# Optimization experiments

Measured on AMD Instinct MI355X. Metric: run time of the kernel, lower is better.

The kernel has to match this reference:

```python
import jax, jax.numpy as jnp
import numpy as np

VOCAB = 50257
EMB = 256
HID = 256
B = 128
S = 2048


def setup_inputs() -> dict:
    key = jax.random.key(0)
    ks = jax.random.split(key, 18)
    w = 0.05  # weight scale to keep tanh/sigmoid in a sane range
    return {
        "x": jax.random.randint(ks[0], (B,), 0, VOCAB),
        "encoder_states": jax.random.normal(ks[1], (S, B, HID), jnp.float32),
        "hidden": jax.random.normal(ks[2], (1, B, HID), jnp.float32),
        "cell": jax.random.normal(ks[3], (1, B, HID), jnp.float32),
        "emb_table": jax.random.normal(ks[4], (VOCAB, EMB), jnp.float32) * w,
        "W_ih": jax.random.normal(ks[5], (4 * HID, EMB + HID), jnp.float32) * w,
        "W_hh": jax.random.normal(ks[6], (4 * HID, HID), jnp.float32) * w,
        "b_ih": jax.random.normal(ks[7], (4 * HID,), jnp.float32) * w,
        "b_hh": jax.random.normal(ks[8], (4 * HID,), jnp.float32) * w,
        "fc_w": jax.random.normal(ks[9], (VOCAB, HID), jnp.float32) * w,
        "fc_b": jax.random.normal(ks[10], (VOCAB,), jnp.float32) * w,
        "W1_w": jax.random.normal(ks[11], (HID, HID), jnp.float32) * w,
        "W1_b": jax.random.normal(ks[12], (HID,), jnp.float32) * w,
        "W2_w": jax.random.normal(ks[13], (HID, HID), jnp.float32) * w,
        "W2_b": jax.random.normal(ks[14], (HID,), jnp.float32) * w,
        "V_w": jax.random.normal(ks[15], (1, HID), jnp.float32) * w,
        "V_b": jax.random.normal(ks[16], (1,), jnp.float32) * w,
    }


def reference(x, encoder_states, hidden, cell, emb_table, W_ih, W_hh, b_ih, b_hh,
              fc_w, fc_b, W1_w, W1_b, W2_w, W2_b, V_w, V_b):
    # encoder_states: [S, B, H] -> [B, S, H]
    enc = jnp.transpose(encoder_states, (1, 0, 2))
    h0 = hidden[0]  # [B, H]  (num_layers == 1)
    c0 = cell[0]

    # Bahdanau additive attention
    score = jnp.tanh(enc @ W1_w.T + W1_b + (h0 @ W2_w.T + W2_b)[:, None, :])  # [B,S,H]
    attw = jax.nn.softmax(score @ V_w.T + V_b, axis=1)  # [B, S, 1]
    ctx = jnp.sum(attw * enc, axis=1)  # [B, H]

    # embedding (dropout is identity in eval/deterministic mode)
    emb = emb_table[x]  # [B, E]
    rnn_in = jnp.concatenate([ctx, emb], axis=-1)  # [B, H+E]

    # single LSTM step; PyTorch gate order: i, f, g, o
    gates = rnn_in @ W_ih.T + b_ih + h0 @ W_hh.T + b_hh  # [B, 4H]
    i, f, g, o = jnp.split(gates, 4, axis=-1)
    c_new = jax.nn.sigmoid(f) * c0 + jax.nn.sigmoid(i) * jnp.tanh(g)
    h_new = jax.nn.sigmoid(o) * jnp.tanh(c_new)

    predictions = h_new @ fc_w.T + fc_b  # [B, VOCAB]
    return predictions, h_new[None], c_new[None], attw
```

## Files before the change

kernel.cpp:

```cpp
#include <hip/hip_runtime.h>
#include <hip/hip_bf16.h>

#define VOCAB 50257
#define EMB 256
#define HID 256
#define BB 128
#define SS 2048

typedef __attribute__((ext_vector_type(8))) short short8;
typedef __attribute__((ext_vector_type(4))) float f32x4;

__device__ inline unsigned short f2bf(float f) {
    unsigned int u = __float_as_uint(f);
    u += 0x7FFFu + ((u >> 16) & 1u);
    return (unsigned short)(u >> 16);
}
__device__ inline unsigned int pack2(float a, float b) {
    return (unsigned int)f2bf(a) | ((unsigned int)f2bf(b) << 16);
}
__device__ inline uint4 pack8(float4 a, float4 b) {
    return make_uint4(pack2(a.x, a.y), pack2(a.z, a.w), pack2(b.x, b.y), pack2(b.z, b.w));
}
__device__ inline float fast_tanh(float x) {
    x = fminf(fmaxf(x, -9.f), 9.f);
    float t = __expf(2.f * x);
    return (t - 1.f) * __builtin_amdgcn_rcpf(t + 1.f);
}

__global__ __launch_bounds__(256) void k_prep(
    const float* __restrict__ hidden, const float* __restrict__ W2,
    const float* __restrict__ W1bias, const float* __restrict__ W2bias,
    const float* __restrict__ W1, unsigned short* __restrict__ W1bf,
    float* __restrict__ qb)
{
    const int bid = blockIdx.x, tid = threadIdx.x;
    if (bid < BB) {
        __shared__ float h0s[HID];
        h0s[tid] = hidden[bid * HID + tid];
        __syncthreads();
        const float4* w2r = (const float4*)(W2 + (size_t)tid * HID);
        float acc = W1bias[tid] + W2bias[tid];
        #pragma unroll 4
        for (int k4 = 0; k4 < HID / 4; ++k4) {
            float4 w = w2r[k4];
            acc += w.x * h0s[k4*4] + w.y * h0s[k4*4+1] + w.z * h0s[k4*4+2] + w.w * h0s[k4*4+3];
        }
        qb[bid * HID + tid] = acc;
    } else {
        int idx = (bid - BB) * 256 + tid;
        float4 v = ((const float4*)W1)[idx];
        ushort4 o;
        o.x = f2bf(v.x); o.y = f2bf(v.y); o.z = f2bf(v.z); o.w = f2bf(v.w);
        ((ushort4*)W1bf)[idx] = o;
    }
}

__global__ __launch_bounds__(512, 2) void k_escore(
    const float* __restrict__ enc, const unsigned short* __restrict__ W1bf,
    const float* __restrict__ qb, const float* __restrict__ Vw,
    const float* __restrict__ Vb, float* __restrict__ e)
{
    __shared__ __align__(16) char As[256 * 128];
    __shared__ __align__(16) char Bs[256 * 128];
    __shared__ float esum[256];

    const int tid = threadIdx.x;
    const int lane = tid & 63, wid = tid >> 6;
    const int wm = wid >> 1, wn = wid & 1;
    const int lg = lane >> 4, li = lane & 15;
    const size_t row0 = (size_t)blockIdx.x * 256;

    if (tid < 256) esum[tid] = 0.f;

    f32x4 acc[4][8];
    #pragma unroll
    for (int m = 0; m < 4; ++m)
        #pragma unroll
        for (int n = 0; n < 8; ++n)
            acc[m][n] = (f32x4){0.f, 0.f, 0.f, 0.f};

    const int a_k16 = tid & 15, a_row0 = tid >> 4;
    const int b_k8 = tid & 7, b_col0 = tid >> 3;

    for (int kt = 0; kt < 4; ++kt) {
        __syncthreads();
        #pragma unroll
        for (int i = 0; i < 8; ++i) {
            const int row = a_row0 + 32 * i;
            float4 v = *((const float4*)(enc + (row0 + row) * HID + kt * 64) + a_k16);
            uint2 p = make_uint2(pack2(v.x, v.y), pack2(v.z, v.w));
            *(uint2*)(As + row * 128 + ((a_k16 * 8) ^ ((row & 7) << 4))) = p;
        }
        #pragma unroll
        for (int i = 0; i < 4; ++i) {
            const int col = b_col0 + 64 * i;
            uint4 v = *((const uint4*)(W1bf + (size_t)col * HID + kt * 64) + b_k8);
            *(uint4*)(Bs + col * 128 + ((b_k8 * 16) ^ ((col & 7) << 4))) = v;
        }
        __syncthreads();
        #pragma unroll
        for (int ks = 0; ks < 2; ++ks) {
            short8 a[4];
            #pragma unroll
            for (int m = 0; m < 4; ++m) {
                const int r = wm * 64 + m * 16 + li;
                a[m] = *(const short8*)(As + r * 128 + ((ks * 64 + lg * 16) ^ ((r & 7) << 4)));
            }
            #pragma unroll
            for (int n = 0; n < 8; ++n) {
                const int c = wn * 128 + n * 16 + li;
                short8 b = *(const short8*)(Bs + c * 128 + ((ks * 64 + lg * 16) ^ ((c & 7) << 4)));
                #pragma unroll
                for (int m = 0; m < 4; ++m)
                    acc[m][n] = __builtin_amdgcn_mfma_f32_16x16x32_bf16(a[m], b, acc[m][n], 0, 0, 0);
            }
        }
    }

    float vw[8];
    #pragma unroll
    for (int n = 0; n < 8; ++n) vw[n] = Vw[wn * 128 + n * 16 + li];

    #pragma unroll
    for (int m = 0; m < 4; ++m) {
        #pragma unroll
        for (int r = 0; r < 4; ++r) {
            const int lrow = wm * 64 + m * 16 + lg * 4 + r;
            const size_t g = row0 + lrow;
            const float* qbrow = qb + (size_t)(g & 127) * HID;
            float p = 0.f;
            #pragma unroll
            for (int n = 0; n < 8; ++n) {
                const int h = wn * 128 + n * 16 + li;
                p += vw[n] * fast_tanh(acc[m][n][r] + qbrow[h]);
            }
            p += __shfl_xor(p, 1); p += __shfl_xor(p, 2);
            p += __shfl_xor(p, 4); p += __shfl_xor(p, 8);
            if (li == 0) atomicAdd(&esum[lrow], p);
        }
    }
    __syncthreads();
    if (tid < 256) {
        const size_t g = row0 + tid;
        e[(size_t)(g & 127) * SS + (g >> 7)] = esum[tid] + Vb[0];
    }
}

__global__ __launch_bounds__(256) void k_softmax(
    const float* __restrict__ e, float* __restrict__ attw)
{
    __shared__ float redm[4];
    __shared__ float reds[4];
    const int b = blockIdx.x, tid = threadIdx.x;
    const float* er = e + (size_t)b * SS;
    float v[8];
    float m = -1e30f;
    #pragma unroll
    for (int i = 0; i < 8; ++i) { v[i] = er[tid + i * 256]; m = fmaxf(m, v[i]); }
    #pragma unroll
    for (int off = 1; off < 64; off <<= 1) m = fmaxf(m, __shfl_xor(m, off));
    if ((tid & 63) == 0) redm[tid >> 6] = m;
    __syncthreads();
    m = fmaxf(fmaxf(redm[0], redm[1]), fmaxf(redm[2], redm[3]));
    float sum = 0.f;
    #pragma unroll
    for (int i = 0; i < 8; ++i) { v[i] = __expf(v[i] - m); sum += v[i]; }
    #pragma unroll
    for (int off = 1; off < 64; off <<= 1) sum += __shfl_xor(sum, off);
    if ((tid & 63) == 0) reds[tid >> 6] = sum;
    __syncthreads();
    const float inv = 1.f / (reds[0] + reds[1] + reds[2] + reds[3]);
    float* aw = attw + (size_t)b * SS;
    #pragma unroll
    for (int i = 0; i < 8; ++i) aw[tid + i * 256] = v[i] * inv;
}

__global__ __launch_bounds__(256) void k_ctx(
    const float* __restrict__ enc, const float* __restrict__ attw,
    float* __restrict__ ctx)
{
    __shared__ float aws[256];
    __shared__ f32x4 red[256];
    const int b = blockIdx.x >> 3, chunk = blockIdx.x & 7, tid = threadIdx.x;
    const int s0 = chunk * 256;
    const int hq = tid & 63, sg = tid >> 6;
    aws[tid] = attw[(size_t)b * SS + s0 + tid];
    __syncthreads();
    const f32x4* base = (const f32x4*)enc + ((size_t)s0 * BB + b) * 64 + hq;
    f32x4 acc = (f32x4){0.f, 0.f, 0.f, 0.f};
    #pragma unroll 8
    for (int i = 0; i < 64; ++i) {
        const int sl = sg + i * 4;
        f32x4 v = base[(size_t)sl * (BB * HID / 4)];
        acc += v * aws[sl];
    }
    red[tid] = acc;
    __syncthreads();
    if (tid < 64) {
        f32x4 r = red[tid] + red[tid + 64] + red[tid + 128] + red[tid + 192];
        #pragma unroll
        for (int j = 0; j < 4; ++j)
            atomicAdd(&ctx[b * HID + tid * 4 + j], r[j]);
    }
}

__global__ __launch_bounds__(256) void k_lstm(
    const float* __restrict__ ctx, const int* __restrict__ x,
    const float* __restrict__ emb_table, const float* __restrict__ hidden,
    const float* __restrict__ cell,
    const float* __restrict__ W_ih, const float* __restrict__ W_hh,
    const float* __restrict__ b_ih, const float* __restrict__ b_hh,
    float* __restrict__ out_h, float* __restrict__ out_c)
{
    __shared__ float rin[768];
    __shared__ float gates[1024];
    const int b = blockIdx.x, tid = threadIdx.x;
    rin[tid]       = ctx[b * HID + tid];
    rin[256 + tid] = emb_table[(size_t)x[b] * EMB + tid];
    rin[512 + tid] = hidden[b * HID + tid];
    __syncthreads();
    #pragma unroll
    for (int jj = 0; jj < 4; ++jj) {
        const int j = jj * 256 + tid;
        float acc = b_ih[j] + b_hh[j];
        const float4* wi = (const float4*)(W_ih + (size_t)j * 512);
        #pragma unroll 4
        for (int k4 = 0; k4 < 128; ++k4) {
            float4 w = wi[k4];
            acc += w.x*rin[k4*4] + w.y*rin[k4*4+1] + w.z*rin[k4*4+2] + w.w*rin[k4*4+3];
        }
        const float4* wh = (const float4*)(W_hh + (size_t)j * 256);
        #pragma unroll 4
        for (int k4 = 0; k4 < 64; ++k4) {
            float4 w = wh[k4];
            acc += w.x*rin[512+k4*4] + w.y*rin[512+k4*4+1] + w.z*rin[512+k4*4+2] + w.w*rin[512+k4*4+3];
        }
        gates[j] = acc;
    }
    __syncthreads();
    const float ig = gates[tid], fg = gates[256 + tid];
    const float gg = gates[512 + tid], og = gates[768 + tid];
    const float c0 = cell[b * HID + tid];
    const float si = 1.f / (1.f + __expf(-ig));
    const float sf = 1.f / (1.f + __expf(-fg));
    const float so = 1.f / (1.f + __expf(-og));
    const float cn = sf * c0 + si * tanhf(gg);
    const float hn = so * tanhf(cn);
    out_c[b * HID + tid] = cn;
    out_h[b * HID + tid] = hn;
}

__global__ __launch_bounds__(256, 2) void k_fc(
    const float* __restrict__ hnew, const float* __restrict__ fcw,
    const float* __restrict__ fcb, float* __restrict__ pred)
{
    __shared__ __align__(16) char As[128 * 64];
    __shared__ __align__(16) char Bs[128 * 64];
    const int vbase = blockIdx.x * 128;
    const int tid = threadIdx.x;
    const int lane = tid & 63, wid = tid >> 6;
    const int wm = wid >> 1, wn = wid & 1;
    const int lg = lane >> 4, li = lane & 15;

    f32x4 acc[4][4];
    #pragma unroll
    for (int m = 0; m < 4; ++m)
        #pragma unroll
        for (int n = 0; n < 4; ++n)
            acc[m][n] = (f32x4){0.f, 0.f, 0.f, 0.f};

    const int arow = tid >> 1, ahalf = tid & 1;
    const float* aptr = hnew + (size_t)arow * HID + ahalf * 16;
    char* awr0 = As + arow * 64 + ((ahalf * 32)      ^ ((arow & 3) << 4));
    char* awr1 = As + arow * 64 + ((ahalf * 32 + 16) ^ ((arow & 3) << 4));
    const int bcol = arow;
    const int v = vbase + bcol;
    const bool vok = v < VOCAB;
    const float* bptr = fcw + (size_t)v * HID + ahalf * 16;
    char* bwr0 = Bs + bcol * 64 + ((ahalf * 32)      ^ ((bcol & 3) << 4));
    char* bwr1 = Bs + bcol * 64 + ((ahalf * 32 + 16) ^ ((bcol & 3) << 4));

    int a_off[4], b_off[4];
    #pragma unroll
    for (int m = 0; m < 4; ++m) { int r = wm*64 + m*16 + li; a_off[m] = r*64 + ((lg*16) ^ ((r&3)<<4)); }
    #pragma unroll
    for (int n = 0; n < 4; ++n) { int c = wn*64 + n*16 + li; b_off[n] = c*64 + ((lg*16) ^ ((c&3)<<4)); }

    for (int kt = 0; kt < 8; ++kt) {
        __syncthreads();
        const float4* ap = (const float4*)(aptr + kt * 32);
        float4 f0 = ap[0], f1 = ap[1], f2 = ap[2], f3 = ap[3];
        *(uint4*)awr0 = pack8(f0, f1);
        *(uint4*)awr1 = pack8(f2, f3);
        float4 g0, g1, g2, g3;
        if (vok) {
            const float4* bp = (const float4*)(bptr + kt * 32);
            g0 = bp[0]; g1 = bp[1]; g2 = bp[2]; g3 = bp[3];
        } else {
            g0 = g1 = g2 = g3 = make_float4(0.f, 0.f, 0.f, 0.f);
        }
        *(uint4*)bwr0 = pack8(g0, g1);
        *(uint4*)bwr1 = pack8(g2, g3);
        __syncthreads();
        short8 a[4];
        #pragma unroll
        for (int m = 0; m < 4; ++m) a[m] = *(const short8*)(As + a_off[m]);
        #pragma unroll
        for (int n = 0; n < 4; ++n) {
            short8 b = *(const short8*)(Bs + b_off[n]);
            #pragma unroll
            for (int m = 0; m < 4; ++m)
                acc[m][n] = __builtin_amdgcn_mfma_f32_16x16x32_bf16(a[m], b, acc[m][n], 0, 0, 0);
        }
    }

    #pragma unroll
    for (int m = 0; m < 4; ++m)
        #pragma unroll
        for (int r = 0; r < 4; ++r) {
            const int row = wm*64 + m*16 + lg*4 + r;
            #pragma unroll
            for (int n = 0; n < 4; ++n) {
                const int col = vbase + wn*64 + n*16 + li;
                if (col < VOCAB)
                    pred[(size_t)row * VOCAB + col] = acc[m][n][r] + fcb[col];
            }
        }
}

extern "C" void kernel_launch(void* const* d_in, const int* in_sizes, int n_in,
                              void* d_out, int out_size, void* d_ws, size_t ws_size,
                              hipStream_t stream)
{
    const int*   x      = (const int*)  d_in[0];
    const float* enc    = (const float*)d_in[1];
    const float* hidden = (const float*)d_in[2];
    const float* cell   = (const float*)d_in[3];
    const float* emb    = (const float*)d_in[4];
    const float* W_ih   = (const float*)d_in[5];
    const float* W_hh   = (const float*)d_in[6];
    const float* b_ih   = (const float*)d_in[7];
    const float* b_hh   = (const float*)d_in[8];
    const float* fc_w   = (const float*)d_in[9];
    const float* fc_b   = (const float*)d_in[10];
    const float* W1_w   = (const float*)d_in[11];
    const float* W1_b   = (const float*)d_in[12];
    const float* W2_w   = (const float*)d_in[13];
    const float* W2_b   = (const float*)d_in[14];
    const float* V_w    = (const float*)d_in[15];
    const float* V_b    = (const float*)d_in[16];

    float* out   = (float*)d_out;
    float* pred  = out;
    float* out_h = out + (size_t)BB * VOCAB;
    float* out_c = out_h + BB * HID;
    float* attw  = out_c + BB * HID;

    char* ws = (char*)d_ws;
    unsigned short* W1bf = (unsigned short*)ws;
    float* qb  = (float*)(ws + 131072);
    float* e   = (float*)(ws + 262144);
    float* ctx = (float*)(ws + 262144 + 1048576);

    k_prep   <<<dim3(192),               dim3(256), 0, stream>>>(hidden, W2_w, W1_b, W2_b, W1_w, W1bf, qb);
    k_escore <<<dim3(1024),              dim3(512), 0, stream>>>(enc, W1bf, qb, V_w, V_b, e);
    k_softmax<<<dim3(BB),                dim3(256), 0, stream>>>(e, attw);
    hipMemsetAsync(ctx, 0, BB * HID * sizeof(float), stream);
    k_ctx    <<<dim3(BB * 8),            dim3(256), 0, stream>>>(enc, attw, ctx);
    k_lstm   <<<dim3(BB),                dim3(256), 0, stream>>>(ctx, x, emb, hidden, cell,
                                                                 W_ih, W_hh, b_ih, b_hh, out_h, out_c);
    k_fc     <<<dim3((VOCAB + 127)/128), dim3(256), 0, stream>>>(out_h, fc_w, fc_b, pred);
}
```

Measured before the change: 682.5 us.

## Retile attention-score and FC GEMMs with register prefetch, finer ctx split, bf16 hidden

The attention-score kernel moves from 256-row, 512-thread blocks to 64-row, 256-thread blocks and writes scores in [S,B] layout, which the softmax now reads strided. Both the score and FC GEMMs prefetch the next K tile into registers while the current tile is computed, and the FC kernel uses 64-wide K tiles over 4 steps instead of 32-wide over 8. The LSTM kernel also writes a bf16 copy of h so the FC loads A without converting it. The ctx reduction is split into 16 chunks per batch row instead of 8, and the tanh clamp is dropped with a cheaper formula. The goal is more blocks in flight and global-load latency hidden behind MFMA work, at the cost of more registers per thread and a strided softmax read.

```diff
diff --git a/kernel.cpp b/kernel.cpp
--- a/kernel.cpp
+++ b/kernel.cpp
@@ -18,13 +18,9 @@
 __device__ inline unsigned int pack2(float a, float b) {
     return (unsigned int)f2bf(a) | ((unsigned int)f2bf(b) << 16);
 }
-__device__ inline uint4 pack8(float4 a, float4 b) {
-    return make_uint4(pack2(a.x, a.y), pack2(a.z, a.w), pack2(b.x, b.y), pack2(b.z, b.w));
-}
 __device__ inline float fast_tanh(float x) {
-    x = fminf(fmaxf(x, -9.f), 9.f);
     float t = __expf(2.f * x);
-    return (t - 1.f) * __builtin_amdgcn_rcpf(t + 1.f);
+    return 1.f - 2.f * __builtin_amdgcn_rcpf(t + 1.f);
 }
 
 __global__ __launch_bounds__(256) void k_prep(
@@ -55,83 +51,107 @@
     }
 }
 
-__global__ __launch_bounds__(512, 2) void k_escore(
+__global__ __launch_bounds__(256) void k_escore(
     const float* __restrict__ enc, const unsigned short* __restrict__ W1bf,
     const float* __restrict__ qb, const float* __restrict__ Vw,
-    const float* __restrict__ Vb, float* __restrict__ e)
-{
-    __shared__ __align__(16) char As[256 * 128];
+    const float* __restrict__ Vb, float* __restrict__ e2)
+{
+    __shared__ __align__(16) char As[64 * 128];
     __shared__ __align__(16) char Bs[256 * 128];
-    __shared__ float esum[256];
+    __shared__ float esum[64];
 
     const int tid = threadIdx.x;
-    const int lane = tid & 63, wid = tid >> 6;
-    const int wm = wid >> 1, wn = wid & 1;
+    const int lane = tid & 63, wn = tid >> 6;
     const int lg = lane >> 4, li = lane & 15;
-    const size_t row0 = (size_t)blockIdx.x * 256;
-
-    if (tid < 256) esum[tid] = 0.f;
-
-    f32x4 acc[4][8];
+    const int blk = blockIdx.x;
+    const size_t row0 = (size_t)blk * 64;
+
+    if (tid < 64) esum[tid] = 0.f;
+
+    f32x4 acc[4][4];
     #pragma unroll
     for (int m = 0; m < 4; ++m)
         #pragma unroll
-        for (int n = 0; n < 8; ++n)
+        for (int n = 0; n < 4; ++n)
             acc[m][n] = (f32x4){0.f, 0.f, 0.f, 0.f};
 
-    const int a_k16 = tid & 15, a_row0 = tid >> 4;
-    const int b_k8 = tid & 7, b_col0 = tid >> 3;
-
-    for (int kt = 0; kt < 4; ++kt) {
-        __syncthreads();
+    float4 ar[4];
+    uint4  br[8];
+
+    auto load_tile = [&](int kt) {
+        #pragma unroll
+        for (int i = 0; i < 4; ++i) {
+            const int slot = tid + 256 * i;
+            const int row = slot >> 4, k16 = slot & 15;
+            ar[i] = *(const float4*)(enc + (row0 + row) * HID + kt * 64 + k16 * 4);
+        }
         #pragma unroll
         for (int i = 0; i < 8; ++i) {
-            const int row = a_row0 + 32 * i;
-            float4 v = *((const float4*)(enc + (row0 + row) * HID + kt * 64) + a_k16);
-            uint2 p = make_uint2(pack2(v.x, v.y), pack2(v.z, v.w));
-            *(uint2*)(As + row * 128 + ((a_k16 * 8) ^ ((row & 7) << 4))) = p;
-        }
+            const int slot = tid + 256 * i;
+            const int col = slot >> 3, k8 = slot & 7;
+            br[i] = *((const uint4*)(W1bf + (size_t)col * HID + kt * 64) + k8);
+        }
+    };
+    auto write_tile = [&]() {
         #pragma unroll
         for (int i = 0; i < 4; ++i) {
-            const int col = b_col0 + 64 * i;
-            uint4 v = *((const uint4*)(W1bf + (size_t)col * HID + kt * 64) + b_k8);
-            *(uint4*)(Bs + col * 128 + ((b_k8 * 16) ^ ((col & 7) << 4))) = v;
-        }
-        __syncthreads();
+            const int slot = tid + 256 * i;
+            const int row = slot >> 4, k16 = slot & 15;
+            *(uint2*)(As + row * 128 + ((k16 * 8) ^ ((row & 7) << 4))) =
+                make_uint2(pack2(ar[i].x, ar[i].y), pack2(ar[i].z, ar[i].w));
+        }
+        #pragma unroll
+        for (int i = 0; i < 8; ++i) {
+            const int slot = tid + 256 * i;
+            const int col = slot >> 3, k8 = slot & 7;
+            *(uint4*)(Bs + col * 128 + ((k8 * 16) ^ ((col & 7) << 4))) = br[i];
+        }
+    };
+    auto compute_tile = [&]() {
         #pragma unroll
         for (int ks = 0; ks < 2; ++ks) {
             short8 a[4];
             #pragma unroll
             for (int m = 0; m < 4; ++m) {
-                const int r = wm * 64 + m * 16 + li;
+                const int r = m * 16 + li;
                 a[m] = *(const short8*)(As + r * 128 + ((ks * 64 + lg * 16) ^ ((r & 7) << 4)));
             }
             #pragma unroll
-            for (int n = 0; n < 8; ++n) {
-                const int c = wn * 128 + n * 16 + li;
+            for (int n = 0; n < 4; ++n) {
+                const int c = wn * 64 + n * 16 + li;
                 short8 b = *(const short8*)(Bs + c * 128 + ((ks * 64 + lg * 16) ^ ((c & 7) << 4)));
                 #pragma unroll
                 for (int m = 0; m < 4; ++m)
                     acc[m][n] = __builtin_amdgcn_mfma_f32_16x16x32_bf16(a[m], b, acc[m][n], 0, 0, 0);
             }
         }
-    }
-
-    float vw[8];
-    #pragma unroll
-    for (int n = 0; n < 8; ++n) vw[n] = Vw[wn * 128 + n * 16 + li];
-
+    };
+
+    load_tile(0);
+    #pragma unroll
+    for (int kt = 0; kt < 4; ++kt) {
+        __syncthreads();
+        write_tile();
+        __syncthreads();
+        if (kt < 3) load_tile(kt + 1);
+        compute_tile();
+    }
+
+    float vw[4];
+    #pragma unroll
+    for (int n = 0; n < 4; ++n) vw[n] = Vw[wn * 64 + n * 16 + li];
+
+    const int bbase = (blk & 1) * 64;
     #pragma unroll
     for (int m = 0; m < 4; ++m) {
         #pragma unroll
         for (int r = 0; r < 4; ++r) {
-            const int lrow = wm * 64 + m * 16 + lg * 4 + r;
-            const size_t g = row0 + lrow;
-            const float* qbrow = qb + (size_t)(g & 127) * HID;
+            const int lrow = m * 16 + lg * 4 + r;
+            const float* qbrow = qb + (size_t)(bbase + lrow) * HID;
             float p = 0.f;
             #pragma unroll
-            for (int n = 0; n < 8; ++n) {
-                const int h = wn * 128 + n * 16 + li;
+            for (int n = 0; n < 4; ++n) {
+                const int h = wn * 64 + n * 16 + li;
                 p += vw[n] * fast_tanh(acc[m][n][r] + qbrow[h]);
             }
             p += __shfl_xor(p, 1); p += __shfl_xor(p, 2);
@@ -140,23 +160,25 @@
         }
     }
     __syncthreads();
-    if (tid < 256) {
-        const size_t g = row0 + tid;
-        e[(size_t)(g & 127) * SS + (g >> 7)] = esum[tid] + Vb[0];
+    if (tid < 64) {
+        const int s = blk >> 1, b = bbase + tid;
+        e2[(size_t)s * BB + b] = esum[tid] + Vb[0];
     }
 }
 
 __global__ __launch_bounds__(256) void k_softmax(
-    const float* __restrict__ e, float* __restrict__ attw)
+    const float* __restrict__ e2, float* __restrict__ attw)
 {
     __shared__ float redm[4];
     __shared__ float reds[4];
     const int b = blockIdx.x, tid = threadIdx.x;
-    const float* er = e + (size_t)b * SS;
     float v[8];
     float m = -1e30f;
     #pragma unroll
-    for (int i = 0; i < 8; ++i) { v[i] = er[tid + i * 256]; m = fmaxf(m, v[i]); }
+    for (int i = 0; i < 8; ++i) {
+        v[i] = e2[(size_t)(tid + i * 256) * BB + b];
+        m = fmaxf(m, v[i]);
+    }
     #pragma unroll
     for (int off = 1; off < 64; off <<= 1) m = fmaxf(m, __shfl_xor(m, off));
     if ((tid & 63) == 0) redm[tid >> 6] = m;
@@ -179,17 +201,17 @@
     const float* __restrict__ enc, const float* __restrict__ attw,
     float* __restrict__ ctx)
 {
-    __shared__ float aws[256];
+    __shared__ float aws[128];
     __shared__ f32x4 red[256];
-    const int b = blockIdx.x >> 3, chunk = blockIdx.x & 7, tid = threadIdx.x;
-    const int s0 = chunk * 256;
+    const int b = blockIdx.x >> 4, chunk = blockIdx.x & 15, tid = threadIdx.x;
+    const int s0 = chunk * 128;
     const int hq = tid & 63, sg = tid >> 6;
-    aws[tid] = attw[(size_t)b * SS + s0 + tid];
+    if (tid < 128) aws[tid] = attw[(size_t)b * SS + s0 + tid];
     __syncthreads();
     const f32x4* base = (const f32x4*)enc + ((size_t)s0 * BB + b) * 64 + hq;
     f32x4 acc = (f32x4){0.f, 0.f, 0.f, 0.f};
     #pragma unroll 8
-    for (int i = 0; i < 64; ++i) {
+    for (int i = 0; i < 32; ++i) {
         const int sl = sg + i * 4;
         f32x4 v = base[(size_t)sl * (BB * HID / 4)];
         acc += v * aws[sl];
@@ -210,7 +232,8 @@
     const float* __restrict__ cell,
     const float* __restrict__ W_ih, const float* __restrict__ W_hh,
     const float* __restrict__ b_ih, const float* __restrict__ b_hh,
-    float* __restrict__ out_h, float* __restrict__ out_c)
+    float* __restrict__ out_h, float* __restrict__ out_c,
+    unsigned short* __restrict__ hbf)
 {
     __shared__ float rin[768];
     __shared__ float gates[1024];
@@ -248,14 +271,15 @@
     const float hn = so * tanhf(cn);
     out_c[b * HID + tid] = cn;
     out_h[b * HID + tid] = hn;
-}
-
-__global__ __launch_bounds__(256, 2) void k_fc(
-    const float* __restrict__ hnew, const float* __restrict__ fcw,
+    hbf[b * HID + tid] = f2bf(hn);
+}
+
+__global__ __launch_bounds__(256) void k_fc(
+    const unsigned short* __restrict__ hbf, const float* __restrict__ fcw,
     const float* __restrict__ fcb, float* __restrict__ pred)
 {
-    __shared__ __align__(16) char As[128 * 64];
-    __shared__ __align__(16) char Bs[128 * 64];
+    __shared__ __align__(16) char As[128 * 128];
+    __shared__ __align__(16) char Bs[128 * 128];
     const int vbase = blockIdx.x * 128;
     const int tid = threadIdx.x;
     const int lane = tid & 63, wid = tid >> 6;
@@ -269,59 +293,77 @@
         for (int n = 0; n < 4; ++n)
             acc[m][n] = (f32x4){0.f, 0.f, 0.f, 0.f};
 
-    const int arow = tid >> 1, ahalf = tid & 1;
-    const float* aptr = hnew + (size_t)arow * HID + ahalf * 16;
-    char* awr0 = As + arow * 64 + ((ahalf * 32)      ^ ((arow & 3) << 4));
-    char* awr1 = As + arow * 64 + ((ahalf * 32 + 16) ^ ((arow & 3) << 4));
-    const int bcol = arow;
-    const int v = vbase + bcol;
-    const bool vok = v < VOCAB;
-    const float* bptr = fcw + (size_t)v * HID + ahalf * 16;
-    char* bwr0 = Bs + bcol * 64 + ((ahalf * 32)      ^ ((bcol & 3) << 4));
-    char* bwr1 = Bs + bcol * 64 + ((ahalf * 32 + 16) ^ ((bcol & 3) << 4));
-
-    int a_off[4], b_off[4];
-    #pragma unroll
-    for (int m = 0; m < 4; ++m) { int r = wm*64 + m*16 + li; a_off[m] = r*64 + ((lg*16) ^ ((r&3)<<4)); }
-    #pragma unroll
-    for (int n = 0; n < 4; ++n) { int c = wn*64 + n*16 + li; b_off[n] = c*64 + ((lg*16) ^ ((c&3)<<4)); }
-
-    for (int kt = 0; kt < 8; ++kt) {
+    uint4  arg[4];
+    float4 brg[8];
+
+    auto load_tile = [&](int kt) {
+        #pragma unroll
+        for (int i = 0; i < 4; ++i) {
+            const int slot = tid + 256 * i;
+            const int row = slot >> 3, k8 = slot & 7;
+            arg[i] = *((const uint4*)(hbf + (size_t)row * HID + kt * 64) + k8);
+        }
+        #pragma unroll
+        for (int i = 0; i < 8; ++i) {
+            const int slot = tid + 256 * i;
+            const int row = slot >> 4, k16 = slot & 15;
+            const int v = min(vbase + row, VOCAB - 1);
+            brg[i] = *(const float4*)(fcw + (size_t)v * HID + kt * 64 + k16 * 4);
+        }
+    };
+    auto write_tile = [&]() {
+        #pragma unroll
+        for (int i = 0; i < 4; ++i) {
+            const int slot = tid + 256 * i;
+            const int row = slot >> 3, k8 = slot & 7;
+            *(uint4*)(As + row * 128 + ((k8 * 16) ^ ((row & 7) << 4))) = arg[i];
+        }
+        #pragma unroll
+        for (int i = 0; i < 8; ++i) {
+            const int slot = tid + 256 * i;
+            const int row = slot >> 4, k16 = slot & 15;
+            *(uint2*)(Bs + row * 128 + ((k16 * 8) ^ ((row & 7) << 4))) =
+                make_uint2(pack2(brg[i].x, brg[i].y), pack2(brg[i].z, brg[i].w));
+        }
+    };
+    auto compute_tile = [&]() {
+        #pragma unroll
+        for (int ks = 0; ks < 2; ++ks) {
+            short8 a[4];
+            #pragma unroll
+            for (int m = 0; m < 4; ++m) {
+                const int r = wm * 64 + m * 16 + li;
+                a[m] = *(const short8*)(As + r * 128 + ((ks * 64 + lg * 16) ^ ((r & 7) << 4)));
+            }
+            #pragma unroll
+            for (int n = 0; n < 4; ++n) {
+                const int c = wn * 64 + n * 16 + li;
+                short8 b = *(const short8*)(Bs + c * 128 + ((ks * 64 + lg * 16) ^ ((c & 7) << 4)));
+                #pragma unroll
+                for (int m = 0; m < 4; ++m)
+                    acc[m][n] = __builtin_amdgcn_mfma_f32_16x16x32_bf16(a[m], b, acc[m][n], 0, 0, 0);
+            }
+        }
+    };
+
+    load_tile(0);
+    #pragma unroll
+    for (int kt = 0; kt < 4; ++kt) {
         __syncthreads();
-        const float4* ap = (const float4*)(aptr + kt * 32);
-        float4 f0 = ap[0], f1 = ap[1], f2 = ap[2], f3 = ap[3];
-        *(uint4*)awr0 = pack8(f0, f1);
-        *(uint4*)awr1 = pack8(f2, f3);
-        float4 g0, g1, g2, g3;
-        if (vok) {
-            const float4* bp = (const float4*)(bptr + kt * 32);
-            g0 = bp[0]; g1 = bp[1]; g2 = bp[2]; g3 = bp[3];
-        } else {
-            g0 = g1 = g2 = g3 = make_float4(0.f, 0.f, 0.f, 0.f);
-        }
-        *(uint4*)bwr0 = pack8(g0, g1);
-        *(uint4*)bwr1 = pack8(g2, g3);
+        write_tile();
         __syncthreads();
-        short8 a[4];
-        #pragma unroll
-        for (int m = 0; m < 4; ++m) a[m] = *(const short8*)(As + a_off[m]);
-        #pragma unroll
-        for (int n = 0; n < 4; ++n) {
-            short8 b = *(const short8*)(Bs + b_off[n]);
-            #pragma unroll
-            for (int m = 0; m < 4; ++m)
-                acc[m][n] = __builtin_amdgcn_mfma_f32_16x16x32_bf16(a[m], b, acc[m][n], 0, 0, 0);
-        }
+        if (kt < 3) load_tile(kt + 1);
+        compute_tile();
     }
 
     #pragma unroll
     for (int m = 0; m < 4; ++m)
         #pragma unroll
         for (int r = 0; r < 4; ++r) {
-            const int row = wm*64 + m*16 + lg*4 + r;
+            const int row = wm * 64 + m * 16 + lg * 4 + r;
             #pragma unroll
             for (int n = 0; n < 4; ++n) {
-                const int col = vbase + wn*64 + n*16 + li;
+                const int col = vbase + wn * 64 + n * 16 + li;
                 if (col < VOCAB)
                     pred[(size_t)row * VOCAB + col] = acc[m][n][r] + fcb[col];
             }
@@ -359,15 +401,16 @@
     char* ws = (char*)d_ws;
     unsigned short* W1bf = (unsigned short*)ws;
     float* qb  = (float*)(ws + 131072);
-    float* e   = (float*)(ws + 262144);
-    float* ctx = (float*)(ws + 262144 + 1048576);
+    float* e2  = (float*)(ws + 262144);
+    float* ctx = (float*)(ws + 1310720);
+    unsigned short* hbf = (unsigned short*)(ws + 1441792);
 
     k_prep   <<<dim3(192),               dim3(256), 0, stream>>>(hidden, W2_w, W1_b, W2_b, W1_w, W1bf, qb);
-    k_escore <<<dim3(1024),              dim3(512), 0, stream>>>(enc, W1bf, qb, V_w, V_b, e);
-    k_softmax<<<dim3(BB),                dim3(256), 0, stream>>>(e, attw);
+    k_escore <<<dim3(SS * 2),            dim3(256), 0, stream>>>(enc, W1bf, qb, V_w, V_b, e2);
+    k_softmax<<<dim3(BB),                dim3(256), 0, stream>>>(e2, attw);
     hipMemsetAsync(ctx, 0, BB * HID * sizeof(float), stream);
-    k_ctx    <<<dim3(BB * 8),            dim3(256), 0, stream>>>(enc, attw, ctx);
+    k_ctx    <<<dim3(BB * 16),           dim3(256), 0, stream>>>(enc, attw, ctx);
     k_lstm   <<<dim3(BB),                dim3(256), 0, stream>>>(ctx, x, emb, hidden, cell,
-                                                                 W_ih, W_hh, b_ih, b_hh, out_h, out_c);
-    k_fc     <<<dim3((VOCAB + 127)/128), dim3(256), 0, stream>>>(out_h, fc_w, fc_b, pred);
-}
+                                                                 W_ih, W_hh, b_ih, b_hh, out_h, out_c, hbf);
+    k_fc     <<<dim3((VOCAB + 127)/128), dim3(256), 0, stream>>>(hbf, fc_w, fc_b, pred);
+}
```

Result: slower. 894.1 us (+31.0%).
